# Kernel optimization log

Measured on AMD Instinct MI355X. Metric: run time of the kernel, lower is better.

Reference implementation:

```python
import jax, jax.numpy as jnp
import numpy as np

SEGMENT_LENGTHS = (512, 1024, 2048)
DILATION_RATES = (1, 2, 4)


def _dilated_attention(q, k, v):
    """LongNet-style dilated segment attention.

    Faithful to RingDilatedAttentionHybridFixed._fallback_forward (ring_size=1,
    non-causal, eval mode): for each (segment_length, dilation_rate) pair the
    sequence is tiled into segments; queries attend to K/V gathered at strided
    (dilated) positions start + i*dilation within the sequence; indices past
    seq_len are masked out (the torch code drops them). Each group writes the
    full output buffer, so later groups overwrite earlier ones, exactly as in
    the source loop.
    """
    B, N, H, D = q.shape
    scale = D ** -0.5
    out = jnp.zeros_like(q)
    for seg_len, dil in zip(SEGMENT_LENGTHS, DILATION_RATES):
        seg = min(seg_len, N)
        nseg = N // seg  # N chosen divisible by every segment length
        qg = q.reshape(B, nseg, seg, H, D)
        # dilated kv indices per segment: start + i*dilation  -> [nseg, seg]
        idx = (jnp.arange(nseg) * seg)[:, None] + jnp.arange(seg)[None, :] * dil
        valid = idx < N
        idxc = jnp.minimum(idx, N - 1)
        kg = k[:, idxc]  # [B, nseg, seg, H, D]
        vg = v[:, idxc]
        scores = jnp.einsum('bnqhd,bnkhd->bnhqk', qg, kg) * scale
        scores = jnp.where(valid[None, :, None, None, :], scores, -jnp.inf)
        attn = jax.nn.softmax(scores, axis=-1)
        seg_out = jnp.einsum('bnhqk,bnkhd->bnqhd', attn, vg)
        # each group covers all positions -> whole-output overwrite (as in torch)
        out = seg_out.reshape(B, N, H, D)
    return out


def setup_inputs() -> dict:
    key = jax.random.key(0)
    kq, kk, kv = jax.random.split(key, 3)
    B, N, H, D = 1, 4096, 16, 64
    q = jax.random.normal(kq, (B, N, H, D), dtype=jnp.float32)
    k = jax.random.normal(kk, (B, N, H, D), dtype=jnp.float32)
    v = jax.random.normal(kv, (B, N, H, D), dtype=jnp.float32)
    return {"q": q, "k": k, "v": v}


def reference(q, k, v):
    return _dilated_attention(q, k, v)
```

## Files before the change

kernel.cpp:

```cpp
#include <hip/hip_runtime.h>
#include <hip/hip_bf16.h>
#include <stdint.h>


#define NH   16
#define HD   64
#define KMAX 1024
#define KBLK 64

typedef __attribute__((ext_vector_type(8))) short s16x8;
typedef __attribute__((ext_vector_type(4))) short s16x4;
typedef __attribute__((ext_vector_type(4))) float f32x4;

__device__ __forceinline__ uint cvtpk(float lo, float hi) {
    uint r;
    asm("v_cvt_pk_bf16_f32 %0, %1, %2" : "=v"(r) : "v"(lo), "v"(hi));
    return r;
}

__device__ __forceinline__ float fexp2(float x) {
#if __has_builtin(__builtin_amdgcn_exp2f)
    return __builtin_amdgcn_exp2f(x);
#else
    return exp2f(x);
#endif
}

__device__ __forceinline__ void async_load16(const ushort* g, ushort* l) {
    __builtin_amdgcn_global_load_lds(
        (const __attribute__((address_space(1))) void*)g,
        (__attribute__((address_space(3))) void*)l, 16, 0, 0);
}

__global__ __launch_bounds__(256) void prep_kernel(
    const float* __restrict__ kin, const float* __restrict__ vin,
    ushort* __restrict__ Kb, ushort* __restrict__ Vt)
{
    int bid = blockIdx.x;
    int h   = bid >> 4;
    int ib  = bid & 15;
    int i0  = ib * 64;

    int t  = threadIdx.x;
    int il = t >> 2;
    int d0 = (t & 3) * 16;
    int i  = i0 + il;
    int pos = i * 4;

    const float* ks = kin + (size_t)pos * (NH*HD) + h * HD + d0;
    const float* vs = vin + (size_t)pos * (NH*HD) + h * HD + d0;

    union { uint u[8]; ushort s[16]; uint4 q4[2]; } kb, vb;
    #pragma unroll
    for (int j = 0; j < 4; ++j) {
        float4 a = ((const float4*)ks)[j];
        float4 b = ((const float4*)vs)[j];
        kb.u[2*j]   = cvtpk(a.x, a.y);
        kb.u[2*j+1] = cvtpk(a.z, a.w);
        vb.u[2*j]   = cvtpk(b.x, b.y);
        vb.u[2*j+1] = cvtpk(b.z, b.w);
    }
    size_t kdst = ((size_t)h * KMAX + i) * HD + d0;
    ((uint4*)(Kb + kdst))[0] = kb.q4[0];
    ((uint4*)(Kb + kdst))[1] = kb.q4[1];

    __shared__ ushort vl[64 * 72];
    #pragma unroll
    for (int j = 0; j < 16; ++j) vl[il * 72 + d0 + j] = vb.s[j];
    __syncthreads();

    int d  = t >> 2;
    int ic = (t & 3) * 16;
    __attribute__((aligned(16))) ushort ob[16];
    #pragma unroll
    for (int j = 0; j < 16; ++j) ob[j] = vl[(ic + j) * 72 + d];
    size_t vdst = ((size_t)h * HD + d) * KMAX + i0 + ic;
    ((uint4*)(Vt + vdst))[0] = *(const uint4*)&ob[0];
    ((uint4*)(Vt + vdst))[1] = *(const uint4*)&ob[8];
}

__global__ __launch_bounds__(256, 4) void attn_kernel(
    const float* __restrict__ qin, const ushort* __restrict__ Kb,
    const ushort* __restrict__ Vt, float* __restrict__ outp)
{
    int bid = blockIdx.x;
    int h   = bid & 15;
    int qb  = (bid >> 4) & 31;
    int seg = bid >> 9;
    int NT  = seg ? 8 : 16;

    int tid  = threadIdx.x;
    int w    = tid >> 6;
    int lane = tid & 63;
    int r15  = lane & 15;
    int g    = lane >> 4;
    int rsw  = r15 & 7;

    __shared__ __attribute__((aligned(16))) ushort kls[2][KBLK*HD];
    __shared__ __attribute__((aligned(16))) ushort vls[2][HD*KBLK];

    const float QSC = 0.125f * 1.4426950408889634f;
    s16x8 qa0, qa1;
    int qrow = seg*2048 + qb*64 + w*16 + r15;
    {
        const float* qs = qin + (size_t)qrow * (NH*HD) + h*HD + g*8;
        float4 a = ((const float4*)qs)[0];
        float4 b = ((const float4*)qs)[1];
        union { uint u[4]; s16x8 v; } r0;
        r0.u[0] = cvtpk(a.x*QSC, a.y*QSC);
        r0.u[1] = cvtpk(a.z*QSC, a.w*QSC);
        r0.u[2] = cvtpk(b.x*QSC, b.y*QSC);
        r0.u[3] = cvtpk(b.z*QSC, b.w*QSC);
        qa0 = r0.v;
        float4 c = ((const float4*)(qs + 32))[0];
        float4 d = ((const float4*)(qs + 32))[1];
        union { uint u[4]; s16x8 v; } r1;
        r1.u[0] = cvtpk(c.x*QSC, c.y*QSC);
        r1.u[1] = cvtpk(c.z*QSC, c.w*QSC);
        r1.u[2] = cvtpk(d.x*QSC, d.y*QSC);
        r1.u[3] = cvtpk(d.z*QSC, d.w*QSC);
        qa1 = r1.v;
    }

    const ushort* KbH = Kb + ((size_t)h * KMAX + seg*512) * HD;
    const ushort* VtH = Vt + (size_t)h * HD * KMAX + seg*512;
    int sub = lane >> 3;
    int csw = (lane & 7) ^ sub;
    bool isK = (w < 2);
    size_t stride = isK ? (size_t)(KBLK*HD) : (size_t)KBLK;
    const ushort* gsrc[4];
    {
        int clb = (w & 1) * 4;
        #pragma unroll
        for (int cc = 0; cc < 4; ++cc) {
            int cl   = clb + cc;
            int rowl = cl*8 + sub;
            gsrc[cc] = isK ? (KbH + (size_t)rowl*HD   + csw*8)
                           : (VtH + (size_t)rowl*KMAX + csw*8);
        }
    }
    ushort* lb0 = isK ? &kls[0][(w & 1) * 2048] : &vls[0][(w & 1) * 2048];
    ushort* lb1 = isK ? &kls[1][(w & 1) * 2048] : &vls[1][(w & 1) * 2048];

    auto stage = [&](ushort* base, int t) {
        size_t off = (size_t)t * stride;
        #pragma unroll
        for (int cc = 0; cc < 4; ++cc) async_load16(gsrc[cc] + off, base + cc*512);
    };

    f32x4 O[4] = {{0,0,0,0},{0,0,0,0},{0,0,0,0},{0,0,0,0}};
    float l = 0.f;

    auto compute = [&](const ushort* kbuf, const ushort* vbuf) {
        f32x4 st[4];
        __builtin_amdgcn_s_setprio(1);
        #pragma unroll
        for (int tt = 0; tt < 4; ++tt) {
            const ushort* kr = kbuf + (tt*16 + r15) * HD;
            s16x8 a0 = *(const s16x8*)(kr + (( g      ^ rsw) << 3));
            s16x8 a1 = *(const s16x8*)(kr + (((g + 4) ^ rsw) << 3));
            f32x4 z = {0.f,0.f,0.f,0.f};
            z      = __builtin_amdgcn_mfma_f32_16x16x32_bf16(a0, qa0, z, 0,0,0);
            st[tt] = __builtin_amdgcn_mfma_f32_16x16x32_bf16(a1, qa1, z, 0,0,0);
        }
        __builtin_amdgcn_s_setprio(0);

        s16x4 pf[4];
        float rs = 0.f;
        #pragma unroll
        for (int tt = 0; tt < 4; ++tt) {
            float p0 = fexp2(st[tt][0]);
            float p1 = fexp2(st[tt][1]);
            float p2 = fexp2(st[tt][2]);
            float p3 = fexp2(st[tt][3]);
            rs += (p0 + p1) + (p2 + p3);
            union { uint u[2]; s16x4 v; } pv;
            pv.u[0] = cvtpk(p0, p1);
            pv.u[1] = cvtpk(p2, p3);
            pf[tt] = pv.v;
        }
        l += rs;

        __builtin_amdgcn_s_setprio(1);
        #pragma unroll
        for (int dt = 0; dt < 4; ++dt) {
            const ushort* vr = vbuf + (dt*16 + r15) * KBLK;
            #pragma unroll
            for (int tt = 0; tt < 4; ++tt) {
                int c = 2*tt + (g >> 1);
                s16x4 vf = *(const s16x4*)(vr + ((c ^ rsw) << 3) + 4*(g & 1));
                O[dt] = __builtin_amdgcn_mfma_f32_16x16x16bf16_1k(vf, pf[tt], O[dt], 0,0,0);
            }
        }
        __builtin_amdgcn_s_setprio(0);
    };

    stage(lb0, 0);
    asm volatile("s_waitcnt vmcnt(0)" ::: "memory");
    __builtin_amdgcn_s_barrier();

    int t = 0;
    for (;;) {
        if (t + 1 < NT) stage(lb1, t + 1);
        compute(&kls[0][0], &vls[0][0]);
        asm volatile("s_waitcnt lgkmcnt(0)" ::: "memory");
        if (++t == NT) break;
        asm volatile("s_waitcnt vmcnt(0)" ::: "memory");
        __builtin_amdgcn_s_barrier();

        if (t + 1 < NT) stage(lb0, t + 1);
        compute(&kls[1][0], &vls[1][0]);
        asm volatile("s_waitcnt lgkmcnt(0)" ::: "memory");
        if (++t == NT) break;
        asm volatile("s_waitcnt vmcnt(0)" ::: "memory");
        __builtin_amdgcn_s_barrier();
    }

    l += __shfl_xor(l, 16);
    l += __shfl_xor(l, 32);
    float invl = 1.0f / l;
    float* ob = outp + (size_t)qrow * (NH*HD) + h*HD + g*4;
    #pragma unroll
    for (int dt = 0; dt < 4; ++dt) {
        float4 o4 = { O[dt][0]*invl, O[dt][1]*invl, O[dt][2]*invl, O[dt][3]*invl };
        *(float4*)(ob + dt*16) = o4;
    }
}

extern "C" void kernel_launch(void* const* d_in, const int* in_sizes, int n_in,
                              void* d_out, int out_size, void* d_ws, size_t ws_size,
                              hipStream_t stream) {
    const float* q = (const float*)d_in[0];
    const float* k = (const float*)d_in[1];
    const float* v = (const float*)d_in[2];
    float* out = (float*)d_out;

    ushort* Kb = (ushort*)d_ws;
    ushort* Vt = Kb + (size_t)NH * KMAX * HD;

    prep_kernel<<<256, 256, 0, stream>>>(k, v, Kb, Vt);
    attn_kernel<<<1024, 256, 0, stream>>>(q, Kb, Vt, out);
}
```

Before: 33.46 us.

## Split KV range across warp pairs with LDS reduction, smaller blocks, more CTAs

Each block now handles 32 query rows instead of 64. Its four warps are split into two query groups times two KV halves, so each warp pair processes half the keys and the partial outputs and row sums are merged through LDS at the end. The tile shrinks to 32 keys, the grid doubles to 2048 blocks, and launch bounds rise to 6 blocks per CU. This raises parallelism and occupancy, but it drops the double-buffered prefetch in favour of a synchronous load-then-barrier per step and adds a final reduction.

```diff
diff --git a/kernel.cpp b/kernel.cpp
--- a/kernel.cpp
+++ b/kernel.cpp
@@ -6,7 +6,6 @@
 #define NH   16
 #define HD   64
 #define KMAX 1024
-#define KBLK 64
 
 typedef __attribute__((ext_vector_type(8))) short s16x8;
 typedef __attribute__((ext_vector_type(4))) short s16x4;
@@ -79,29 +78,31 @@
     ((uint4*)(Vt + vdst))[1] = *(const uint4*)&ob[8];
 }
 
-__global__ __launch_bounds__(256, 4) void attn_kernel(
+__global__ __launch_bounds__(256, 6) void attn_kernel(
     const float* __restrict__ qin, const ushort* __restrict__ Kb,
     const ushort* __restrict__ Vt, float* __restrict__ outp)
 {
     int bid = blockIdx.x;
     int h   = bid & 15;
-    int qb  = (bid >> 4) & 31;
-    int seg = bid >> 9;
-    int NT  = seg ? 8 : 16;
+    int qb  = (bid >> 4) & 63;
+    int seg = bid >> 10;
+    int NS  = seg ? 8 : 16;
 
     int tid  = threadIdx.x;
-    int w    = tid >> 6;
+    int wid  = tid >> 6;
+    int qg   = wid & 1;
+    int kh   = wid >> 1;
     int lane = tid & 63;
     int r15  = lane & 15;
     int g    = lane >> 4;
     int rsw  = r15 & 7;
 
-    __shared__ __attribute__((aligned(16))) ushort kls[2][KBLK*HD];
-    __shared__ __attribute__((aligned(16))) ushort vls[2][HD*KBLK];
+    __shared__ __attribute__((aligned(16))) ushort kls[2][32*HD];
+    __shared__ __attribute__((aligned(16))) ushort vls[2][HD*32];
 
     const float QSC = 0.125f * 1.4426950408889634f;
     s16x8 qa0, qa1;
-    int qrow = seg*2048 + qb*64 + w*16 + r15;
+    int qrow = seg*2048 + qb*32 + qg*16 + r15;
     {
         const float* qs = qin + (size_t)qrow * (NH*HD) + h*HD + g*8;
         float4 a = ((const float4*)qs)[0];
@@ -122,40 +123,53 @@
         qa1 = r1.v;
     }
 
-    const ushort* KbH = Kb + ((size_t)h * KMAX + seg*512) * HD;
-    const ushort* VtH = Vt + (size_t)h * HD * KMAX + seg*512;
-    int sub = lane >> 3;
-    int csw = (lane & 7) ^ sub;
-    bool isK = (w < 2);
-    size_t stride = isK ? (size_t)(KBLK*HD) : (size_t)KBLK;
+    int kbase = seg*512 + kh*(NS*32);
     const ushort* gsrc[4];
-    {
-        int clb = (w & 1) * 4;
+    size_t gstep;
+    ushort* ldst;
+    if (qg == 0) {
+        const ushort* gK = Kb + ((size_t)h*KMAX + kbase)*HD;
+        int srow = lane >> 3;
+        int pc   = lane & 7;
         #pragma unroll
         for (int cc = 0; cc < 4; ++cc) {
-            int cl   = clb + cc;
-            int rowl = cl*8 + sub;
-            gsrc[cc] = isK ? (KbH + (size_t)rowl*HD   + csw*8)
-                           : (VtH + (size_t)rowl*KMAX + csw*8);
-        }
-    }
-    ushort* lb0 = isK ? &kls[0][(w & 1) * 2048] : &vls[0][(w & 1) * 2048];
-    ushort* lb1 = isK ? &kls[1][(w & 1) * 2048] : &vls[1][(w & 1) * 2048];
-
-    auto stage = [&](ushort* base, int t) {
-        size_t off = (size_t)t * stride;
-        #pragma unroll
-        for (int cc = 0; cc < 4; ++cc) async_load16(gsrc[cc] + off, base + cc*512);
-    };
+            int row = cc*8 + srow;
+            gsrc[cc] = gK + (size_t)row*HD + ((pc ^ (row & 7)) << 3);
+        }
+        gstep = (size_t)(32*HD);
+        ldst  = &kls[kh][0];
+    } else {
+        const ushort* gV = Vt + (size_t)h*HD*KMAX + kbase;
+        int srow = lane >> 2;
+        int pc   = lane & 3;
+        #pragma unroll
+        for (int cc = 0; cc < 4; ++cc) {
+            int row = cc*16 + srow;
+            gsrc[cc] = gV + (size_t)row*KMAX + ((pc ^ (row & 3)) << 3);
+        }
+        gstep = (size_t)32;
+        ldst  = &vls[kh][0];
+    }
 
     f32x4 O[4] = {{0,0,0,0},{0,0,0,0},{0,0,0,0},{0,0,0,0}};
     float l = 0.f;
 
-    auto compute = [&](const ushort* kbuf, const ushort* vbuf) {
-        f32x4 st[4];
-        __builtin_amdgcn_s_setprio(1);
-        #pragma unroll
-        for (int tt = 0; tt < 4; ++tt) {
+    const ushort* kbuf = &kls[kh][0];
+    const ushort* vbuf = &vls[kh][0];
+
+    for (int s = 0; s < NS; ++s) {
+        {
+            size_t off = (size_t)s * gstep;
+            #pragma unroll
+            for (int cc = 0; cc < 4; ++cc)
+                async_load16(gsrc[cc] + off, ldst + cc*512);
+        }
+        asm volatile("s_waitcnt vmcnt(0)" ::: "memory");
+        __builtin_amdgcn_s_barrier();
+
+        f32x4 st[2];
+        #pragma unroll
+        for (int tt = 0; tt < 2; ++tt) {
             const ushort* kr = kbuf + (tt*16 + r15) * HD;
             s16x8 a0 = *(const s16x8*)(kr + (( g      ^ rsw) << 3));
             s16x8 a1 = *(const s16x8*)(kr + (((g + 4) ^ rsw) << 3));
@@ -163,67 +177,59 @@
             z      = __builtin_amdgcn_mfma_f32_16x16x32_bf16(a0, qa0, z, 0,0,0);
             st[tt] = __builtin_amdgcn_mfma_f32_16x16x32_bf16(a1, qa1, z, 0,0,0);
         }
-        __builtin_amdgcn_s_setprio(0);
-
-        s16x4 pf[4];
-        float rs = 0.f;
-        #pragma unroll
-        for (int tt = 0; tt < 4; ++tt) {
+
+        s16x4 pf[2];
+        #pragma unroll
+        for (int tt = 0; tt < 2; ++tt) {
             float p0 = fexp2(st[tt][0]);
             float p1 = fexp2(st[tt][1]);
             float p2 = fexp2(st[tt][2]);
             float p3 = fexp2(st[tt][3]);
-            rs += (p0 + p1) + (p2 + p3);
+            l += (p0 + p1) + (p2 + p3);
             union { uint u[2]; s16x4 v; } pv;
             pv.u[0] = cvtpk(p0, p1);
             pv.u[1] = cvtpk(p2, p3);
             pf[tt] = pv.v;
         }
-        l += rs;
-
-        __builtin_amdgcn_s_setprio(1);
+
         #pragma unroll
         for (int dt = 0; dt < 4; ++dt) {
-            const ushort* vr = vbuf + (dt*16 + r15) * KBLK;
+            const ushort* vr = vbuf + (dt*16 + r15) * 32;
             #pragma unroll
-            for (int tt = 0; tt < 4; ++tt) {
+            for (int tt = 0; tt < 2; ++tt) {
                 int c = 2*tt + (g >> 1);
-                s16x4 vf = *(const s16x4*)(vr + ((c ^ rsw) << 3) + 4*(g & 1));
+                s16x4 vf = *(const s16x4*)(vr + ((c ^ (r15 & 3)) << 3) + 4*(g & 1));
                 O[dt] = __builtin_amdgcn_mfma_f32_16x16x16bf16_1k(vf, pf[tt], O[dt], 0,0,0);
             }
         }
-        __builtin_amdgcn_s_setprio(0);
-    };
-
-    stage(lb0, 0);
-    asm volatile("s_waitcnt vmcnt(0)" ::: "memory");
-    __builtin_amdgcn_s_barrier();
-
-    int t = 0;
-    for (;;) {
-        if (t + 1 < NT) stage(lb1, t + 1);
-        compute(&kls[0][0], &vls[0][0]);
+
         asm volatile("s_waitcnt lgkmcnt(0)" ::: "memory");
-        if (++t == NT) break;
-        asm volatile("s_waitcnt vmcnt(0)" ::: "memory");
-        __builtin_amdgcn_s_barrier();
-
-        if (t + 1 < NT) stage(lb0, t + 1);
-        compute(&kls[1][0], &vls[1][0]);
-        asm volatile("s_waitcnt lgkmcnt(0)" ::: "memory");
-        if (++t == NT) break;
-        asm volatile("s_waitcnt vmcnt(0)" ::: "memory");
         __builtin_amdgcn_s_barrier();
     }
 
     l += __shfl_xor(l, 16);
     l += __shfl_xor(l, 32);
-    float invl = 1.0f / l;
-    float* ob = outp + (size_t)qrow * (NH*HD) + h*HD + g*4;
-    #pragma unroll
-    for (int dt = 0; dt < 4; ++dt) {
-        float4 o4 = { O[dt][0]*invl, O[dt][1]*invl, O[dt][2]*invl, O[dt][3]*invl };
-        *(float4*)(ob + dt*16) = o4;
+
+    float* Op = (float*)&kls[0][0];
+    float* ll = Op + 32*68;
+    int qloc = qg*16 + r15;
+    if (kh == 1) {
+        #pragma unroll
+        for (int dt = 0; dt < 4; ++dt)
+            *(f32x4*)(Op + qloc*68 + dt*16 + g*4) = O[dt];
+        if (g == 0) ll[qloc] = l;
+    }
+    __syncthreads();
+    if (kh == 0) {
+        float invl = 1.0f / (l + ll[qloc]);
+        float* ob = outp + (size_t)qrow * (NH*HD) + h*HD + g*4;
+        #pragma unroll
+        for (int dt = 0; dt < 4; ++dt) {
+            f32x4 p4 = *(const f32x4*)(Op + qloc*68 + dt*16 + g*4);
+            float4 o4 = { (O[dt][0]+p4[0])*invl, (O[dt][1]+p4[1])*invl,
+                          (O[dt][2]+p4[2])*invl, (O[dt][3]+p4[3])*invl };
+            *(float4*)(ob + dt*16) = o4;
+        }
     }
 }
 
@@ -239,5 +245,5 @@
     ushort* Vt = Kb + (size_t)NH * KMAX * HD;
 
     prep_kernel<<<256, 256, 0, stream>>>(k, v, Kb, Vt);
-    attn_kernel<<<1024, 256, 0, stream>>>(q, Kb, Vt, out);
-}
+    attn_kernel<<<2048, 256, 0, stream>>>(q, Kb, Vt, out);
+}
```

After: 46.42 us. +38.7%, slower.
